# Kernel tuning notes

Measured on AMD Instinct MI355X. Metric: run time of the kernel, lower is better.

Reference implementation:

```python
import jax, jax.numpy as jnp
import numpy as np

W_SIZE = 7
C_DIM = 256
HEADS = 8
HEAD_DIM = 32
HIDDEN = 1024
B, H, W = 32, 56, 56


def _rel_pos_index(w):
    coords = np.stack(np.meshgrid(np.arange(w), np.arange(w), indexing='ij'))  # (2,w,w)
    cf = coords.reshape(2, -1)                       # (2, w*w)
    rc = (cf[:, :, None] - cf[:, None, :]).transpose(1, 2, 0)  # (N,N,2)
    rc[:, :, 0] += w - 1
    rc[:, :, 1] += w - 1
    rc[:, :, 0] *= 2 * w - 1
    return rc.sum(-1)  # (N,N) int

REL_IDX = jnp.asarray(_rel_pos_index(W_SIZE))


def setup_inputs() -> dict:
    key = jax.random.key(0)
    ks = jax.random.split(key, 10)
    s = 0.02
    return {
        'x': jax.random.normal(ks[0], (B, H, W, C_DIM), jnp.float32),
        'norm1_g': jnp.ones((C_DIM,), jnp.float32),
        'norm1_b': jnp.zeros((C_DIM,), jnp.float32),
        'qkv_w': jax.random.normal(ks[1], (3 * C_DIM, C_DIM), jnp.float32) * s,
        'qkv_b': jnp.zeros((3 * C_DIM,), jnp.float32),
        'bias_table': jax.random.normal(ks[2], ((2 * W_SIZE - 1) ** 2, HEADS), jnp.float32) * s,
        'proj_w': jax.random.normal(ks[3], (C_DIM, C_DIM), jnp.float32) * s,
        'proj_b': jnp.zeros((C_DIM,), jnp.float32),
        'norm2_g': jnp.ones((C_DIM,), jnp.float32),
        'norm2_b': jnp.zeros((C_DIM,), jnp.float32),
        'ffn_w1': jax.random.normal(ks[4], (HIDDEN, C_DIM), jnp.float32) * s,
        'ffn_b1': jnp.zeros((HIDDEN,), jnp.float32),
        'ffn_w2': jax.random.normal(ks[5], (C_DIM, HIDDEN), jnp.float32) * s,
        'ffn_b2': jnp.zeros((C_DIM,), jnp.float32),
    }


def _ln(x, g, b, eps=1e-5):
    m = jnp.mean(x, -1, keepdims=True)
    v = jnp.mean(jnp.square(x - m), -1, keepdims=True)
    return (x - m) * jax.lax.rsqrt(v + eps) * g + b


def reference(x, norm1_g, norm1_b, qkv_w, qkv_b, bias_table, proj_w, proj_b,
              norm2_g, norm2_b, ffn_w1, ffn_b1, ffn_w2, ffn_b2):
    b, h, w, c = x.shape
    ws = W_SIZE
    n = ws * ws
    scale = HEAD_DIM ** -0.5
    shortcut = x

    y = _ln(x, norm1_g, norm1_b)
    # window partition ('block' mode): (B,H,W,C) -> (B*nW, ws*ws, C)
    y = y.reshape(b, h // ws, ws, w // ws, ws, c).transpose(0, 1, 3, 2, 4, 5)
    y = y.reshape(-1, n, c)
    bw = y.shape[0]  # num_windows * B

    qkv = y @ qkv_w.T + qkv_b                               # (bw, n, 3C)
    qkv = qkv.reshape(bw, n, 3, HEADS, HEAD_DIM).transpose(2, 0, 3, 1, 4)
    q, k, v = qkv[0] * scale, qkv[1], qkv[2]                # (bw, heads, n, d)

    attn = jnp.einsum('bhnd,bhmd->bhnm', q, k)              # (bw, heads, n, n)
    rel_bias = bias_table[REL_IDX].transpose(2, 0, 1)       # (heads, n, n)
    attn = jax.nn.softmax(attn + rel_bias[None], axis=-1)

    o = jnp.einsum('bhnm,bhmd->bhnd', attn, v)              # (bw, heads, n, d)
    o = o.transpose(0, 2, 1, 3).reshape(bw, n, c)
    o = o @ proj_w.T + proj_b

    # window reverse
    o = o.reshape(b, h // ws, w // ws, ws, ws, c).transpose(0, 1, 3, 2, 4, 5)
    o = o.reshape(b, h, w, c)

    x = shortcut + o
    z = _ln(x, norm2_g, norm2_b)
    z = jax.nn.gelu(z @ ffn_w1.T + ffn_b1, approximate=False) @ ffn_w2.T + ffn_b2
    return x + z
```

## Files before the change

### kernel.cpp

```cpp
#include <hip/hip_runtime.h>
#include <math.h>

typedef unsigned short u16;
typedef __attribute__((ext_vector_type(8))) __bf16 bf16x8;
typedef __attribute__((ext_vector_type(8))) u16 u16x8;
typedef __attribute__((ext_vector_type(4))) float f32x4;

__device__ __forceinline__ float b2f(u16 u) {
    union { unsigned int u; float f; } a; a.u = ((unsigned int)u) << 16; return a.f;
}
__device__ __forceinline__ u16 f2b(float f) {
    union { __bf16 h; u16 u; } c; c.h = (__bf16)f; return c.u;
}

__device__ __forceinline__ float gelu_t(float x) {
    float x2 = x * x;
    float u  = x * fmaf(0.0713548162726f, x2, 1.5957691216057308f);
    float e  = __expf(u);
    return x * e * __builtin_amdgcn_rcpf(e + 1.0f);
}

__device__ __forceinline__ int win2spatial(int r) {
    int wid = r / 49;
    int n   = r - wid * 49;
    int b   = wid >> 6;
    int wr  = wid & 63;
    int h   = (wr >> 3) * 7 + n / 7;
    int w   = (wr & 7) * 7 + n % 7;
    return (b * 56 + h) * 56 + w;
}

__device__ __forceinline__ void stage16(const u16* g, u16* l) {
    __builtin_amdgcn_global_load_lds((const __attribute__((address_space(1))) void*)g,
                                     (__attribute__((address_space(3))) void*)l, 16, 0, 0);
}

__global__ __launch_bounds__(256) void cvt_kernel(const float* __restrict__ in,
                                                  u16* __restrict__ out, int n)
{
    int i = (blockIdx.x * 256 + threadIdx.x) * 4;
    if (i < n) {
        float4 v = *reinterpret_cast<const float4*>(in + i);
        ushort4 o;
        o.x = f2b(v.x); o.y = f2b(v.y); o.z = f2b(v.z); o.w = f2b(v.w);
        *reinterpret_cast<ushort4*>(out + i) = o;
    }
}

__global__ __launch_bounds__(256) void bias_prep(const float* __restrict__ btab,
                                                 float* __restrict__ btile)
{
    int head = blockIdx.x;
    for (int idx = threadIdx.x; idx < 4096; idx += 256) {
        int i = idx >> 6, j = idx & 63;
        float v = -1e30f;
        if (i < 49 && j < 49) {
            int di = i / 7 - j / 7 + 6;
            int dj = i % 7 - j % 7 + 6;
            v = btab[(di * 13 + dj) * 8 + head];
        }
        btile[head * 4096 + idx] = v;
    }
}

template<int REORDER, int INBF>
__global__ __launch_bounds__(256) void ln_kernel(const void* __restrict__ inp,
                                                 const float* __restrict__ gw,
                                                 const float* __restrict__ bw,
                                                 u16* __restrict__ outp)
{
    int wave = threadIdx.x >> 6, lane = threadIdx.x & 63;
    int row  = blockIdx.x * 4 + wave;
    int irow = REORDER ? win2spatial(row) : row;

    float v[4];
    if (INBF) {
        ushort4 xx = *reinterpret_cast<const ushort4*>((const u16*)inp + (size_t)irow * 256 + lane * 4);
        v[0] = b2f(xx.x); v[1] = b2f(xx.y); v[2] = b2f(xx.z); v[3] = b2f(xx.w);
    } else {
        float4 xx = *reinterpret_cast<const float4*>((const float*)inp + (size_t)irow * 256 + lane * 4);
        v[0] = xx.x; v[1] = xx.y; v[2] = xx.z; v[3] = xx.w;
    }

    float s = v[0] + v[1] + v[2] + v[3];
    float q = v[0]*v[0] + v[1]*v[1] + v[2]*v[2] + v[3]*v[3];
#pragma unroll
    for (int off = 32; off > 0; off >>= 1) {
        s += __shfl_xor(s, off, 64);
        q += __shfl_xor(q, off, 64);
    }
    float mean = s * (1.0f / 256.0f);
    float var  = q * (1.0f / 256.0f) - mean * mean;
    float rstd = rsqrtf(var + 1e-5f);

    int c = lane * 4;
    ushort4 o;
    o.x = f2b((v[0] - mean) * rstd * gw[c + 0] + bw[c + 0]);
    o.y = f2b((v[1] - mean) * rstd * gw[c + 1] + bw[c + 1]);
    o.z = f2b((v[2] - mean) * rstd * gw[c + 2] + bw[c + 2]);
    o.w = f2b((v[3] - mean) * rstd * gw[c + 3] + bw[c + 3]);
    *reinterpret_cast<ushort4*>(outp + (size_t)row * 256 + c) = o;
}

template<int EPI>
__global__ __launch_bounds__(256) void gemm_kernel(
    const u16* __restrict__ A, const u16* __restrict__ W,
    const float* __restrict__ bias,
    u16* __restrict__ outU, float* __restrict__ outF,
    const float* __restrict__ residF, const u16* __restrict__ residU,
    int N, int K, int nB)
{
    __shared__ char smem[49152];
    u16* sA0 = (u16*)smem;
    u16* sA1 = (u16*)(smem + 16384);
    u16* sB  = (u16*)(smem + 32768);

    int t = threadIdx.x;
    int w = t >> 6, lane = t & 63;
    int quad = lane >> 4, l16 = lane & 15;
    int wm = (w >> 1) * 64, wn = (w & 1) * 64;

    int b = blockIdx.x;
    int xcd = b & 7, g = b >> 3;
    int n_i = g % nB;
    int m_i = (g / nB) * 8 + xcd;
    int n_blk = n_i * 128, m_blk = m_i * 128;

    int srow = t >> 3;
    int scol = ((t & 7) ^ (srow & 7)) * 8;
    const u16* pA = A + (size_t)(m_blk + srow) * K + scol;
    const u16* pB = W + (size_t)(n_blk + srow) * K + scol;
    u16* lA0 = sA0 + w * 512;
    u16* lA1 = sA1 + w * 512;
    u16* lB  = sB  + w * 512;

    f32x4 acc[4][4];
#pragma unroll
    for (int i = 0; i < 4; ++i)
#pragma unroll
        for (int j = 0; j < 4; ++j) acc[i][j] = (f32x4){0.f, 0.f, 0.f, 0.f};

    int nk = K >> 6;

#pragma unroll
    for (int gg = 0; gg < 4; ++gg)
        stage16(pA + (size_t)(gg * 32) * K, lA0 + gg * 2048);

    for (int tt = 0; tt < nk; ++tt) {
        int kb = tt << 6;
        __builtin_amdgcn_s_barrier();
#pragma unroll
        for (int gg = 0; gg < 4; ++gg)
            stage16(pB + (size_t)(gg * 32) * K + kb, lB + gg * 2048);
        if (tt + 1 < nk) {
            u16* lAn = (tt & 1) ? lA0 : lA1;
#pragma unroll
            for (int gg = 0; gg < 4; ++gg)
                stage16(pA + (size_t)(gg * 32) * K + kb + 64, lAn + gg * 2048);
            asm volatile("s_waitcnt vmcnt(4)" ::: "memory");
        } else {
            asm volatile("s_waitcnt vmcnt(0)" ::: "memory");
        }
        __builtin_amdgcn_s_barrier();

        const u16* cA = (tt & 1) ? sA1 : sA0;
#pragma unroll
        for (int q32 = 0; q32 < 2; ++q32) {
            bf16x8 af[4], bfr[4];
            int kc = q32 * 4 + quad;
#pragma unroll
            for (int tm = 0; tm < 4; ++tm) {
                int row = wm + tm * 16 + l16;
                af[tm] = *(const bf16x8*)(cA + (unsigned)(row * 8 + (kc ^ (row & 7))) * 8);
            }
#pragma unroll
            for (int tn = 0; tn < 4; ++tn) {
                int row = wn + tn * 16 + l16;
                bfr[tn] = *(const bf16x8*)(sB + (unsigned)(row * 8 + (kc ^ (row & 7))) * 8);
            }
#pragma unroll
            for (int tm = 0; tm < 4; ++tm)
#pragma unroll
                for (int tn = 0; tn < 4; ++tn)
                    acc[tm][tn] = __builtin_amdgcn_mfma_f32_16x16x32_bf16(af[tm], bfr[tn], acc[tm][tn], 0, 0, 0);
        }
    }

    __syncthreads();
    u16* tp = (u16*)smem + w * 4608;

#pragma unroll
    for (int tm = 0; tm < 4; ++tm)
#pragma unroll
        for (int r = 0; r < 4; ++r) {
            int rowL = tm * 16 + quad * 4 + r;
            int srw = 0;
            if (EPI == 2) srw = win2spatial(m_blk + wm + rowL);
#pragma unroll
            for (int tn = 0; tn < 4; ++tn) {
                int colL = tn * 16 + l16;
                float val = acc[tm][tn][r] + bias[n_blk + wn + colL];
                if (EPI == 1) val = gelu_t(val);
                if (EPI == 2) val += residF[(size_t)srw * 256 + n_blk + wn + colL];
                tp[rowL * 72 + colL] = f2b(val);
            }
        }

#pragma unroll
    for (int it = 0; it < 8; ++it) {
        int rowL = it * 8 + (lane >> 3);
        int chunk = (lane & 7) * 8;
        u16x8 vv = *(const u16x8*)(tp + rowL * 72 + chunk);
        int grow = m_blk + wm + rowL;
        if (EPI == 3) {
            size_t o = (size_t)grow * N + n_blk + wn + chunk;
            u16x8 rr = *(const u16x8*)(residU + o);
            float4 f0, f1;
            f0.x = b2f(vv[0]) + b2f(rr[0]);
            f0.y = b2f(vv[1]) + b2f(rr[1]);
            f0.z = b2f(vv[2]) + b2f(rr[2]);
            f0.w = b2f(vv[3]) + b2f(rr[3]);
            f1.x = b2f(vv[4]) + b2f(rr[4]);
            f1.y = b2f(vv[5]) + b2f(rr[5]);
            f1.z = b2f(vv[6]) + b2f(rr[6]);
            f1.w = b2f(vv[7]) + b2f(rr[7]);
            *reinterpret_cast<float4*>(outF + o)     = f0;
            *reinterpret_cast<float4*>(outF + o + 4) = f1;
        } else if (EPI == 2) {
            *(u16x8*)(outU + (size_t)win2spatial(grow) * 256 + n_blk + wn + chunk) = vv;
        } else {
            *(u16x8*)(outU + (size_t)grow * N + n_blk + wn + chunk) = vv;
        }
    }
}

__global__ __launch_bounds__(64) void attn_kernel(const u16* __restrict__ qkv,
                                                  const float* __restrict__ btile,
                                                  u16* __restrict__ o)
{
    __shared__ u16 vT[32 * 72];
    __shared__ u16 pl[64 * 72];

    int wid = blockIdx.x, head = blockIdx.y;
    int lane = threadIdx.x;
    int quad = lane >> 4, l16 = lane & 15;

    const u16* wbase = qkv + (size_t)wid * 49 * 768;

    {
        unsigned long long* z = (unsigned long long*)vT;
        for (int i = lane; i < 576; i += 64) z[i] = 0ull;
    }

    if (lane < 49) {
#pragma unroll
        for (int c = 0; c < 4; ++c) {
            u16x8 vv = *(const u16x8*)(wbase + (size_t)lane * 768 + 512 + head * 32 + c * 8);
#pragma unroll
            for (int i = 0; i < 8; ++i) vT[(c * 8 + i) * 72 + lane] = vv[i];
        }
    }

    bf16x8 aq[4], bk[4];
#pragma unroll
    for (int t = 0; t < 4; ++t) {
        int r = t * 16 + l16; r = r > 48 ? 48 : r;
        aq[t] = *(const bf16x8*)(wbase + (size_t)r * 768 + head * 32 + quad * 8);
        bk[t] = *(const bf16x8*)(wbase + (size_t)r * 768 + 256 + head * 32 + quad * 8);
    }

    f32x4 s[4][4];
#pragma unroll
    for (int tm = 0; tm < 4; ++tm)
#pragma unroll
        for (int tn = 0; tn < 4; ++tn)
            s[tm][tn] = __builtin_amdgcn_mfma_f32_16x16x32_bf16(aq[tm], bk[tn],
                        (f32x4){0.f, 0.f, 0.f, 0.f}, 0, 0, 0);

    const float scale = 0.17677669529663687f;
    const float* bt = btile + head * 4096;
#pragma unroll
    for (int tm = 0; tm < 4; ++tm)
#pragma unroll
        for (int tn = 0; tn < 4; ++tn)
#pragma unroll
            for (int r = 0; r < 4; ++r) {
                float bb = bt[(tm * 16 + quad * 4 + r) * 64 + tn * 16 + l16];
                s[tm][tn][r] = s[tm][tn][r] * scale + bb;
            }

#pragma unroll
    for (int tm = 0; tm < 4; ++tm)
#pragma unroll
        for (int r = 0; r < 4; ++r) {
            float mx = fmaxf(fmaxf(s[tm][0][r], s[tm][1][r]), fmaxf(s[tm][2][r], s[tm][3][r]));
#pragma unroll
            for (int off = 1; off < 16; off <<= 1) mx = fmaxf(mx, __shfl_xor(mx, off, 64));
            float sum = 0.f;
#pragma unroll
            for (int tn = 0; tn < 4; ++tn) {
                float e = __expf(s[tm][tn][r] - mx);
                s[tm][tn][r] = e; sum += e;
            }
#pragma unroll
            for (int off = 1; off < 16; off <<= 1) sum += __shfl_xor(sum, off, 64);
            float inv = 1.0f / sum;
#pragma unroll
            for (int tn = 0; tn < 4; ++tn) s[tm][tn][r] *= inv;
        }

    __syncthreads();
#pragma unroll
    for (int tm = 0; tm < 4; ++tm)
#pragma unroll
        for (int tn = 0; tn < 4; ++tn)
#pragma unroll
            for (int r = 0; r < 4; ++r)
                pl[(tm * 16 + quad * 4 + r) * 72 + tn * 16 + l16] = f2b(s[tm][tn][r]);
    __syncthreads();

    f32x4 oa[4][2];
#pragma unroll
    for (int tm = 0; tm < 4; ++tm)
#pragma unroll
        for (int tn = 0; tn < 2; ++tn) oa[tm][tn] = (f32x4){0.f, 0.f, 0.f, 0.f};

#pragma unroll
    for (int ks = 0; ks < 2; ++ks) {
        bf16x8 pa[4], vb[2];
#pragma unroll
        for (int tm = 0; tm < 4; ++tm)
            pa[tm] = *(const bf16x8*)(pl + (unsigned)(tm * 16 + l16) * 72 + ks * 32 + quad * 8);
#pragma unroll
        for (int tn = 0; tn < 2; ++tn)
            vb[tn] = *(const bf16x8*)(vT + (unsigned)(tn * 16 + l16) * 72 + ks * 32 + quad * 8);
#pragma unroll
        for (int tm = 0; tm < 4; ++tm)
#pragma unroll
            for (int tn = 0; tn < 2; ++tn)
                oa[tm][tn] = __builtin_amdgcn_mfma_f32_16x16x32_bf16(pa[tm], vb[tn], oa[tm][tn], 0, 0, 0);
    }

    u16* ob = o + (size_t)wid * 49 * 256 + head * 32;
#pragma unroll
    for (int tm = 0; tm < 4; ++tm)
#pragma unroll
        for (int r = 0; r < 4; ++r) {
            int m = tm * 16 + quad * 4 + r;
            if (m < 49) {
#pragma unroll
                for (int tn = 0; tn < 2; ++tn)
                    ob[(size_t)m * 256 + tn * 16 + l16] = f2b(oa[tm][tn][r]);
            }
        }
}

extern "C" void kernel_launch(void* const* d_in, const int* in_sizes, int n_in,
                              void* d_out, int out_size, void* d_ws, size_t ws_size,
                              hipStream_t stream)
{
    const float* x     = (const float*)d_in[0];
    const float* n1g   = (const float*)d_in[1];
    const float* n1b   = (const float*)d_in[2];
    const float* qkvw  = (const float*)d_in[3];
    const float* qkvb  = (const float*)d_in[4];
    const float* btab  = (const float*)d_in[5];
    const float* projw = (const float*)d_in[6];
    const float* projb = (const float*)d_in[7];
    const float* n2g   = (const float*)d_in[8];
    const float* n2b   = (const float*)d_in[9];
    const float* w1    = (const float*)d_in[10];
    const float* b1    = (const float*)d_in[11];
    const float* w2    = (const float*)d_in[12];
    const float* b2    = (const float*)d_in[13];

    char* ws  = (char*)d_ws;
    u16* x1   = (u16*)ws;
    u16* bufA = (u16*)(ws + 102760448);
    u16* bufB = (u16*)(ws + 102760448 + 205520896);
    u16* wq   = (u16*)(ws + 102760448 + 205520896 + 51380224);
    u16* wp   = wq + 196608;
    u16* wf1  = wp + 65536;
    u16* wf2  = wf1 + 262144;
    float* btile = (float*)(ws + 102760448 + 154140672);

    cvt_kernel<<<192, 256, 0, stream>>>(qkvw, wq, 196608);
    cvt_kernel<<<64,  256, 0, stream>>>(projw, wp, 65536);
    cvt_kernel<<<256, 256, 0, stream>>>(w1, wf1, 262144);
    cvt_kernel<<<256, 256, 0, stream>>>(w2, wf2, 262144);
    bias_prep<<<8, 256, 0, stream>>>(btab, btile);

    ln_kernel<1, 0><<<25088, 256, 0, stream>>>(x, n1g, n1b, bufB);
    gemm_kernel<0><<<6 * 784, 256, 0, stream>>>(bufB, wq, qkvb, bufA, nullptr,
                                                nullptr, nullptr, 768, 256, 6);
    attn_kernel<<<dim3(2048, 8), 64, 0, stream>>>(bufA, btile, bufB);
    gemm_kernel<2><<<2 * 784, 256, 0, stream>>>(bufB, wp, projb, x1, nullptr,
                                                x, nullptr, 256, 256, 2);
    ln_kernel<0, 1><<<25088, 256, 0, stream>>>(x1, n2g, n2b, bufB);
    gemm_kernel<1><<<8 * 784, 256, 0, stream>>>(bufB, wf1, b1, bufA, nullptr,
                                                nullptr, nullptr, 1024, 256, 8);
    gemm_kernel<3><<<2 * 784, 256, 0, stream>>>(bufA, wf2, b2, nullptr, (float*)d_out,
                                                nullptr, x1, 256, 1024, 2);
}
```

Before: 563.7 us.

## Enlarge GEMM tiles to 256x256 with 16 waves and double-buffered A and B

```diff
diff --git a/kernel.cpp b/kernel.cpp
--- a/kernel.cpp
+++ b/kernel.cpp
@@ -103,36 +103,35 @@
 }
 
 template<int EPI>
-__global__ __launch_bounds__(256) void gemm_kernel(
+__global__ __launch_bounds__(1024) void gemm_kernel(
     const u16* __restrict__ A, const u16* __restrict__ W,
     const float* __restrict__ bias,
     u16* __restrict__ outU, float* __restrict__ outF,
     const float* __restrict__ residF, const u16* __restrict__ residU,
     int N, int K, int nB)
 {
-    __shared__ char smem[49152];
-    u16* sA0 = (u16*)smem;
-    u16* sA1 = (u16*)(smem + 16384);
-    u16* sB  = (u16*)(smem + 32768);
+    __shared__ char smem[131072];
 
     int t = threadIdx.x;
     int w = t >> 6, lane = t & 63;
     int quad = lane >> 4, l16 = lane & 15;
-    int wm = (w >> 1) * 64, wn = (w & 1) * 64;
+    int wm = (w >> 2) * 64, wn = (w & 3) * 64;
 
     int b = blockIdx.x;
     int xcd = b & 7, g = b >> 3;
     int n_i = g % nB;
     int m_i = (g / nB) * 8 + xcd;
-    int n_blk = n_i * 128, m_blk = m_i * 128;
+    int n_blk = n_i * 256, m_blk = m_i * 256;
 
     int srow = t >> 3;
     int scol = ((t & 7) ^ (srow & 7)) * 8;
     const u16* pA = A + (size_t)(m_blk + srow) * K + scol;
     const u16* pB = W + (size_t)(n_blk + srow) * K + scol;
-    u16* lA0 = sA0 + w * 512;
-    u16* lA1 = sA1 + w * 512;
-    u16* lB  = sB  + w * 512;
+
+    u16* lA0 = (u16*)smem + w * 512;
+    u16* lA1 = (u16*)(smem + 32768) + w * 512;
+    u16* lB0 = (u16*)(smem + 65536) + w * 512;
+    u16* lB1 = (u16*)(smem + 98304) + w * 512;
 
     f32x4 acc[4][4];
 #pragma unroll
@@ -142,28 +141,31 @@
 
     int nk = K >> 6;
 
-#pragma unroll
-    for (int gg = 0; gg < 4; ++gg)
-        stage16(pA + (size_t)(gg * 32) * K, lA0 + gg * 2048);
+    {
+        stage16(pA, lA0);
+        stage16(pA + 128 * K, lA0 + 8192);
+        stage16(pB, lB0);
+        stage16(pB + 128 * K, lB0 + 8192);
+    }
 
     for (int tt = 0; tt < nk; ++tt) {
-        int kb = tt << 6;
-        __builtin_amdgcn_s_barrier();
-#pragma unroll
-        for (int gg = 0; gg < 4; ++gg)
-            stage16(pB + (size_t)(gg * 32) * K + kb, lB + gg * 2048);
         if (tt + 1 < nk) {
-            u16* lAn = (tt & 1) ? lA0 : lA1;
-#pragma unroll
-            for (int gg = 0; gg < 4; ++gg)
-                stage16(pA + (size_t)(gg * 32) * K + kb + 64, lAn + gg * 2048);
+            int kb = (tt + 1) << 6;
+            u16* dA = (tt & 1) ? lA0 : lA1;
+            u16* dB = (tt & 1) ? lB0 : lB1;
+            stage16(pA + kb, dA);
+            stage16(pA + 128 * K + kb, dA + 8192);
+            stage16(pB + kb, dB);
+            stage16(pB + 128 * K + kb, dB + 8192);
             asm volatile("s_waitcnt vmcnt(4)" ::: "memory");
         } else {
             asm volatile("s_waitcnt vmcnt(0)" ::: "memory");
         }
         __builtin_amdgcn_s_barrier();
 
-        const u16* cA = (tt & 1) ? sA1 : sA0;
+        const u16* cA = (const u16*)smem + ((tt & 1) ? 16384 : 0);
+        const u16* cB = (const u16*)(smem + 65536) + ((tt & 1) ? 16384 : 0);
+
 #pragma unroll
         for (int q32 = 0; q32 < 2; ++q32) {
             bf16x8 af[4], bfr[4];
@@ -176,7 +178,7 @@
 #pragma unroll
             for (int tn = 0; tn < 4; ++tn) {
                 int row = wn + tn * 16 + l16;
-                bfr[tn] = *(const bf16x8*)(sB + (unsigned)(row * 8 + (kc ^ (row & 7))) * 8);
+                bfr[tn] = *(const bf16x8*)(cB + (unsigned)(row * 8 + (kc ^ (row & 7))) * 8);
             }
 #pragma unroll
             for (int tm = 0; tm < 4; ++tm)
@@ -184,52 +186,58 @@
                 for (int tn = 0; tn < 4; ++tn)
                     acc[tm][tn] = __builtin_amdgcn_mfma_f32_16x16x32_bf16(af[tm], bfr[tn], acc[tm][tn], 0, 0, 0);
         }
+        __builtin_amdgcn_s_barrier();
     }
 
     __syncthreads();
-    u16* tp = (u16*)smem + w * 4608;
-
-#pragma unroll
-    for (int tm = 0; tm < 4; ++tm)
-#pragma unroll
-        for (int r = 0; r < 4; ++r) {
-            int rowL = tm * 16 + quad * 4 + r;
-            int srw = 0;
-            if (EPI == 2) srw = win2spatial(m_blk + wm + rowL);
-#pragma unroll
-            for (int tn = 0; tn < 4; ++tn) {
-                int colL = tn * 16 + l16;
-                float val = acc[tm][tn][r] + bias[n_blk + wn + colL];
-                if (EPI == 1) val = gelu_t(val);
-                if (EPI == 2) val += residF[(size_t)srw * 256 + n_blk + wn + colL];
-                tp[rowL * 72 + colL] = f2b(val);
-            }
-        }
-
-#pragma unroll
-    for (int it = 0; it < 8; ++it) {
-        int rowL = it * 8 + (lane >> 3);
-        int chunk = (lane & 7) * 8;
-        u16x8 vv = *(const u16x8*)(tp + rowL * 72 + chunk);
-        int grow = m_blk + wm + rowL;
-        if (EPI == 3) {
-            size_t o = (size_t)grow * N + n_blk + wn + chunk;
-            u16x8 rr = *(const u16x8*)(residU + o);
-            float4 f0, f1;
-            f0.x = b2f(vv[0]) + b2f(rr[0]);
-            f0.y = b2f(vv[1]) + b2f(rr[1]);
-            f0.z = b2f(vv[2]) + b2f(rr[2]);
-            f0.w = b2f(vv[3]) + b2f(rr[3]);
-            f1.x = b2f(vv[4]) + b2f(rr[4]);
-            f1.y = b2f(vv[5]) + b2f(rr[5]);
-            f1.z = b2f(vv[6]) + b2f(rr[6]);
-            f1.w = b2f(vv[7]) + b2f(rr[7]);
-            *reinterpret_cast<float4*>(outF + o)     = f0;
-            *reinterpret_cast<float4*>(outF + o + 4) = f1;
-        } else if (EPI == 2) {
-            *(u16x8*)(outU + (size_t)win2spatial(grow) * 256 + n_blk + wn + chunk) = vv;
-        } else {
-            *(u16x8*)(outU + (size_t)grow * N + n_blk + wn + chunk) = vv;
+    u16* tp = (u16*)smem + w * 2304;
+
+#pragma unroll
+    for (int p = 0; p < 2; ++p) {
+#pragma unroll
+        for (int tm2 = 0; tm2 < 2; ++tm2) {
+            int tm = p * 2 + tm2;
+#pragma unroll
+            for (int r = 0; r < 4; ++r) {
+                int rowL = tm2 * 16 + quad * 4 + r;
+                int growp = m_blk + wm + p * 32 + rowL;
+                int srw = 0;
+                if (EPI == 2) srw = win2spatial(growp);
+#pragma unroll
+                for (int tn = 0; tn < 4; ++tn) {
+                    int colL = tn * 16 + l16;
+                    float val = acc[tm][tn][r] + bias[n_blk + wn + colL];
+                    if (EPI == 1) val = gelu_t(val);
+                    if (EPI == 2) val += residF[(size_t)srw * 256 + n_blk + wn + colL];
+                    tp[rowL * 72 + colL] = f2b(val);
+                }
+            }
+        }
+#pragma unroll
+        for (int it = 0; it < 4; ++it) {
+            int rowL = it * 8 + (lane >> 3);
+            int chunk = (lane & 7) * 8;
+            u16x8 vv = *(const u16x8*)(tp + rowL * 72 + chunk);
+            int grow = m_blk + wm + p * 32 + rowL;
+            if (EPI == 3) {
+                size_t o = (size_t)grow * N + n_blk + wn + chunk;
+                u16x8 rr = *(const u16x8*)(residU + o);
+                float4 f0, f1;
+                f0.x = b2f(vv[0]) + b2f(rr[0]);
+                f0.y = b2f(vv[1]) + b2f(rr[1]);
+                f0.z = b2f(vv[2]) + b2f(rr[2]);
+                f0.w = b2f(vv[3]) + b2f(rr[3]);
+                *reinterpret_cast<float4*>(outF + o) = f0;
+                f1.x = b2f(vv[4]) + b2f(rr[4]);
+                f1.y = b2f(vv[5]) + b2f(rr[5]);
+                f1.z = b2f(vv[6]) + b2f(rr[6]);
+                f1.w = b2f(vv[7]) + b2f(rr[7]);
+                *reinterpret_cast<float4*>(outF + o + 4) = f1;
+            } else if (EPI == 2) {
+                *(u16x8*)(outU + (size_t)win2spatial(grow) * 256 + n_blk + wn + chunk) = vv;
+            } else {
+                *(u16x8*)(outU + (size_t)grow * N + n_blk + wn + chunk) = vv;
+            }
         }
     }
 }
@@ -391,14 +399,14 @@
     bias_prep<<<8, 256, 0, stream>>>(btab, btile);
 
     ln_kernel<1, 0><<<25088, 256, 0, stream>>>(x, n1g, n1b, bufB);
-    gemm_kernel<0><<<6 * 784, 256, 0, stream>>>(bufB, wq, qkvb, bufA, nullptr,
-                                                nullptr, nullptr, 768, 256, 6);
+    gemm_kernel<0><<<3 * 392, 1024, 0, stream>>>(bufB, wq, qkvb, bufA, nullptr,
+                                                 nullptr, nullptr, 768, 256, 3);
     attn_kernel<<<dim3(2048, 8), 64, 0, stream>>>(bufA, btile, bufB);
-    gemm_kernel<2><<<2 * 784, 256, 0, stream>>>(bufB, wp, projb, x1, nullptr,
-                                                x, nullptr, 256, 256, 2);
+    gemm_kernel<2><<<1 * 392, 1024, 0, stream>>>(bufB, wp, projb, x1, nullptr,
+                                                 x, nullptr, 256, 256, 1);
     ln_kernel<0, 1><<<25088, 256, 0, stream>>>(x1, n2g, n2b, bufB);
-    gemm_kernel<1><<<8 * 784, 256, 0, stream>>>(bufB, wf1, b1, bufA, nullptr,
-                                                nullptr, nullptr, 1024, 256, 8);
-    gemm_kernel<3><<<2 * 784, 256, 0, stream>>>(bufA, wf2, b2, nullptr, (float*)d_out,
-                                                nullptr, x1, 256, 1024, 2);
-}
+    gemm_kernel<1><<<4 * 392, 1024, 0, stream>>>(bufB, wf1, b1, bufA, nullptr,
+                                                 nullptr, nullptr, 1024, 256, 4);
+    gemm_kernel<3><<<1 * 392, 1024, 0, stream>>>(bufA, wf2, b2, nullptr, (float*)d_out,
+                                                 nullptr, x1, 256, 1024, 1);
+}
```

After: 587.9 us. 1.04x slower.

## Load GEMM B fragments directly into registers and template K for full unroll

Applied to the files above, without the earlier changes.

```diff
diff --git a/kernel.cpp b/kernel.cpp
--- a/kernel.cpp
+++ b/kernel.cpp
@@ -102,18 +102,16 @@
     *reinterpret_cast<ushort4*>(outp + (size_t)row * 256 + c) = o;
 }
 
-template<int EPI>
-__global__ __launch_bounds__(256) void gemm_kernel(
+template<int EPI, int NK>
+__global__ __launch_bounds__(256, 3) void gemm_kernel(
     const u16* __restrict__ A, const u16* __restrict__ W,
     const float* __restrict__ bias,
     u16* __restrict__ outU, float* __restrict__ outF,
     const float* __restrict__ residF, const u16* __restrict__ residU,
-    int N, int K, int nB)
-{
-    __shared__ char smem[49152];
-    u16* sA0 = (u16*)smem;
-    u16* sA1 = (u16*)(smem + 16384);
-    u16* sB  = (u16*)(smem + 32768);
+    int N, int nB)
+{
+    constexpr int K = NK * 64;
+    __shared__ char smem[36864];
 
     int t = threadIdx.x;
     int w = t >> 6, lane = t & 63;
@@ -129,10 +127,10 @@
     int srow = t >> 3;
     int scol = ((t & 7) ^ (srow & 7)) * 8;
     const u16* pA = A + (size_t)(m_blk + srow) * K + scol;
-    const u16* pB = W + (size_t)(n_blk + srow) * K + scol;
-    u16* lA0 = sA0 + w * 512;
-    u16* lA1 = sA1 + w * 512;
-    u16* lB  = sB  + w * 512;
+    u16* lA0 = (u16*)smem + w * 512;
+    u16* lA1 = (u16*)(smem + 16384) + w * 512;
+
+    const u16* pB = W + (size_t)(n_blk + wn + l16) * K + quad * 8;
 
     f32x4 acc[4][4];
 #pragma unroll
@@ -140,33 +138,33 @@
 #pragma unroll
         for (int j = 0; j < 4; ++j) acc[i][j] = (f32x4){0.f, 0.f, 0.f, 0.f};
 
-    int nk = K >> 6;
-
+    bf16x8 bbuf[8];
+
+#pragma unroll
+    for (int j = 0; j < 8; ++j)
+        bbuf[j] = *(const bf16x8*)(pB + (size_t)(j >> 1) * 16 * K + (j & 1) * 32);
 #pragma unroll
     for (int gg = 0; gg < 4; ++gg)
         stage16(pA + (size_t)(gg * 32) * K, lA0 + gg * 2048);
 
-    for (int tt = 0; tt < nk; ++tt) {
-        int kb = tt << 6;
-        __builtin_amdgcn_s_barrier();
-#pragma unroll
-        for (int gg = 0; gg < 4; ++gg)
-            stage16(pB + (size_t)(gg * 32) * K + kb, lB + gg * 2048);
-        if (tt + 1 < nk) {
-            u16* lAn = (tt & 1) ? lA0 : lA1;
+#pragma unroll
+    for (int tt = 0; tt < NK; ++tt) {
+        if (tt + 1 < NK) {
+            u16* dA = ((tt + 1) & 1) ? lA1 : lA0;
 #pragma unroll
             for (int gg = 0; gg < 4; ++gg)
-                stage16(pA + (size_t)(gg * 32) * K + kb + 64, lAn + gg * 2048);
+                stage16(pA + (size_t)(gg * 32) * K + (tt + 1) * 64, dA + gg * 2048);
             asm volatile("s_waitcnt vmcnt(4)" ::: "memory");
         } else {
             asm volatile("s_waitcnt vmcnt(0)" ::: "memory");
         }
         __builtin_amdgcn_s_barrier();
-
-        const u16* cA = (tt & 1) ? sA1 : sA0;
+        __builtin_amdgcn_sched_barrier(0);
+
+        const u16* cA = (const u16*)smem + ((tt & 1) ? 8192 : 0);
 #pragma unroll
         for (int q32 = 0; q32 < 2; ++q32) {
-            bf16x8 af[4], bfr[4];
+            bf16x8 af[4];
             int kc = q32 * 4 + quad;
 #pragma unroll
             for (int tm = 0; tm < 4; ++tm) {
@@ -174,16 +172,20 @@
                 af[tm] = *(const bf16x8*)(cA + (unsigned)(row * 8 + (kc ^ (row & 7))) * 8);
             }
 #pragma unroll
-            for (int tn = 0; tn < 4; ++tn) {
-                int row = wn + tn * 16 + l16;
-                bfr[tn] = *(const bf16x8*)(sB + (unsigned)(row * 8 + (kc ^ (row & 7))) * 8);
-            }
-#pragma unroll
             for (int tm = 0; tm < 4; ++tm)
 #pragma unroll
                 for (int tn = 0; tn < 4; ++tn)
-                    acc[tm][tn] = __builtin_amdgcn_mfma_f32_16x16x32_bf16(af[tm], bfr[tn], acc[tm][tn], 0, 0, 0);
-        }
+                    acc[tm][tn] = __builtin_amdgcn_mfma_f32_16x16x32_bf16(
+                        af[tm], bbuf[tn * 2 + q32], acc[tm][tn], 0, 0, 0);
+            if (tt + 1 < NK) {
+#pragma unroll
+                for (int tn = 0; tn < 4; ++tn)
+                    bbuf[tn * 2 + q32] = *(const bf16x8*)(
+                        pB + (size_t)tn * 16 * K + q32 * 32 + (tt + 1) * 64);
+            }
+        }
+        __builtin_amdgcn_sched_barrier(0);
+        __builtin_amdgcn_s_barrier();
     }
 
     __syncthreads();
@@ -220,11 +222,11 @@
             f0.y = b2f(vv[1]) + b2f(rr[1]);
             f0.z = b2f(vv[2]) + b2f(rr[2]);
             f0.w = b2f(vv[3]) + b2f(rr[3]);
+            *reinterpret_cast<float4*>(outF + o) = f0;
             f1.x = b2f(vv[4]) + b2f(rr[4]);
             f1.y = b2f(vv[5]) + b2f(rr[5]);
             f1.z = b2f(vv[6]) + b2f(rr[6]);
             f1.w = b2f(vv[7]) + b2f(rr[7]);
-            *reinterpret_cast<float4*>(outF + o)     = f0;
             *reinterpret_cast<float4*>(outF + o + 4) = f1;
         } else if (EPI == 2) {
             *(u16x8*)(outU + (size_t)win2spatial(grow) * 256 + n_blk + wn + chunk) = vv;
@@ -391,14 +393,14 @@
     bias_prep<<<8, 256, 0, stream>>>(btab, btile);
 
     ln_kernel<1, 0><<<25088, 256, 0, stream>>>(x, n1g, n1b, bufB);
-    gemm_kernel<0><<<6 * 784, 256, 0, stream>>>(bufB, wq, qkvb, bufA, nullptr,
-                                                nullptr, nullptr, 768, 256, 6);
+    gemm_kernel<0, 4><<<6 * 784, 256, 0, stream>>>(bufB, wq, qkvb, bufA, nullptr,
+                                                   nullptr, nullptr, 768, 6);
     attn_kernel<<<dim3(2048, 8), 64, 0, stream>>>(bufA, btile, bufB);
-    gemm_kernel<2><<<2 * 784, 256, 0, stream>>>(bufB, wp, projb, x1, nullptr,
-                                                x, nullptr, 256, 256, 2);
+    gemm_kernel<2, 4><<<2 * 784, 256, 0, stream>>>(bufB, wp, projb, x1, nullptr,
+                                                   x, nullptr, 256, 2);
     ln_kernel<0, 1><<<25088, 256, 0, stream>>>(x1, n2g, n2b, bufB);
-    gemm_kernel<1><<<8 * 784, 256, 0, stream>>>(bufB, wf1, b1, bufA, nullptr,
-                                                nullptr, nullptr, 1024, 256, 8);
-    gemm_kernel<3><<<2 * 784, 256, 0, stream>>>(bufA, wf2, b2, nullptr, (float*)d_out,
-                                                nullptr, x1, 256, 1024, 2);
-}
+    gemm_kernel<1, 4><<<8 * 784, 256, 0, stream>>>(bufB, wf1, b1, bufA, nullptr,
+                                                   nullptr, nullptr, 1024, 8);
+    gemm_kernel<3, 16><<<2 * 784, 256, 0, stream>>>(bufA, wf2, b2, nullptr, (float*)d_out,
+                                                    nullptr, x1, 256, 2);
+}
```

Result: slower. 694.8 us (+23.3%).
